# Kernel optimization log

Measured on AMD Instinct MI355X. Metric: run time of the kernel, lower is better.

## Reference

```python
import jax, jax.numpy as jnp
import numpy as np

IN_CH, D, K = 256, 128, 512

def setup_inputs() -> dict:
    key = jax.random.key(0)
    k1, k2, k3, k4 = jax.random.split(key, 4)
    x = jax.random.normal(k1, (16, IN_CH, 64, 64), dtype=jnp.float32)
    W = jax.random.normal(k2, (D, IN_CH), dtype=jnp.float32) * (1.0 / np.sqrt(IN_CH))
    b = jax.random.normal(k3, (D,), dtype=jnp.float32) * 0.01
    prototypes = jax.random.normal(k4, (K, D), dtype=jnp.float32) * 0.02
    gamma = jnp.asarray(1.0, dtype=jnp.float32)
    return {"x": x, "W": W, "b": b, "prototypes": prototypes, "gamma": gamma}

def reference(x, W, b, prototypes, gamma):
    n, c, h, w = x.shape
    # 1x1 conv projection: [n,c,h,w] -> [n,h,w,d]
    q = jnp.einsum('nchw,dc->nhwd', x, W) + b
    q_flat = q.reshape(n * h * w, -1)                      # [T, d]
    q_norm2 = jnp.sum(q_flat * q_flat, axis=1, keepdims=True)   # [T, 1]
    p_norm2 = jnp.sum(prototypes * prototypes, axis=1)[None, :] # [1, K]
    dist2 = q_norm2 + p_norm2 - 2.0 * (q_flat @ prototypes.T)   # [T, K]
    weights = jax.nn.softmax(-jnp.abs(gamma) * dist2, axis=1)
    return weights.reshape(n, h, w, -1).transpose(0, 3, 1, 2)   # [n, K, h, w]
```

## Files before the change

### kernel.cpp

```cpp
#include <hip/hip_runtime.h>

#define HW 4096
#define NCH 256
#define DIM 128
#define NPROTO 512

typedef __attribute__((ext_vector_type(4))) float f32x4;
typedef __attribute__((ext_vector_type(8))) short s16x8;

__device__ __forceinline__ unsigned short f2bf(float f) {
  union { float f; unsigned u; } v; v.f = f;
  unsigned r = v.u + 0x7fffu + ((v.u >> 16) & 1u);
  return (unsigned short)(r >> 16);
}

__device__ __forceinline__ void gload_lds16(const void* g, void* l) {
  __builtin_amdgcn_global_load_lds(
      (const __attribute__((address_space(1))) void*)g,
      (__attribute__((address_space(3))) void*)l, 16, 0, 0);
}

__global__ __launch_bounds__(256) void prep_kernel(const float* __restrict__ P,
                                                   const float* __restrict__ Wm,
                                                   unsigned short* __restrict__ Pbf,
                                                   unsigned short* __restrict__ Wbf,
                                                   float* __restrict__ pn2) {
  const int tid = threadIdx.x;
  const int b = blockIdx.x;
  if (b < 8) {
    const int n  = b * 64 + (tid >> 2);
    const int qt = tid & 3;
    const float* row = P + n * DIM + qt * 32;
    unsigned short* dst = Pbf + (size_t)n * DIM + qt * 32;
    float ssq = 0.f;
#pragma unroll
    for (int u = 0; u < 8; ++u) {
      f32x4 v = *(const f32x4*)(row + 4 * u);
      ssq += v.x * v.x + v.y * v.y + v.z * v.z + v.w * v.w;
      dst[4 * u + 0] = f2bf(v.x);
      dst[4 * u + 1] = f2bf(v.y);
      dst[4 * u + 2] = f2bf(v.z);
      dst[4 * u + 3] = f2bf(v.w);
    }
    ssq += __shfl_xor(ssq, 1);
    ssq += __shfl_xor(ssq, 2);
    if (qt == 0) pn2[n] = ssq;
  } else {
    const int idx = ((b - 8) * 256 + tid) * 16;
#pragma unroll
    for (int u = 0; u < 4; ++u) {
      f32x4 v = *(const f32x4*)(Wm + idx + 4 * u);
      unsigned short* d = Wbf + idx + 4 * u;
      d[0] = f2bf(v.x); d[1] = f2bf(v.y); d[2] = f2bf(v.z); d[3] = f2bf(v.w);
    }
  }
}

__global__ __launch_bounds__(512) void proj_kernel(const float* __restrict__ x,
                                                   const unsigned short* __restrict__ Wbf,
                                                   const float* __restrict__ bias,
                                                   unsigned short* __restrict__ qbf) {
  __shared__ __align__(16) unsigned short x_s[128 * 72];
  __shared__ __align__(16) unsigned short w_s[128 * 64];
  const int tid  = threadIdx.x;
  const int p0   = blockIdx.x * 128;
  const int nimg = p0 >> 12;
  const int hw0  = p0 & 4095;
  const float* xbase = x + (size_t)nimg * NCH * HW + hw0;
  const int wave = tid >> 6, lane = tid & 63;
  const int l15 = lane & 15, l4 = lane >> 4;

  f32x4 acc[8];
#pragma unroll
  for (int j = 0; j < 8; ++j)
#pragma unroll
    for (int r = 0; r < 4; ++r) acc[j][r] = 0.f;

  const int wrow0 = 8 * wave + (lane >> 3);
  const int wc8   = lane & 7;

  for (int c0 = 0; c0 < NCH; c0 += 64) {
#pragma unroll
    for (int t = 0; t < 2; ++t) {
      const int row = 64 * t + wrow0;
      const unsigned short* src =
          Wbf + (size_t)row * NCH + c0 + ((wc8 ^ (row & 7)) << 3);
      gload_lds16(src, (char*)w_s + t * 8192 + wave * 1024);
    }
    {
      const int f = tid & 31, cl = tid >> 5;
#pragma unroll
      for (int r = 0; r < 4; ++r) {
        const int cc = cl + 16 * r;
        f32x4 v = *(const f32x4*)(xbase + (size_t)(c0 + cc) * HW + 4 * f);
        x_s[(4 * f + 0) * 72 + cc] = f2bf(v.x);
        x_s[(4 * f + 1) * 72 + cc] = f2bf(v.y);
        x_s[(4 * f + 2) * 72 + cc] = f2bf(v.z);
        x_s[(4 * f + 3) * 72 + cc] = f2bf(v.w);
      }
    }
    __syncthreads();
#pragma unroll
    for (int kc = 0; kc < 64; kc += 32) {
      s16x8 a = *(const s16x8*)&x_s[(16 * wave + l15) * 72 + kc + 8 * l4];
      const int ub = (kc >> 3) + l4;
#pragma unroll
      for (int j = 0; j < 8; ++j) {
        s16x8 b = *(const s16x8*)&w_s[(16 * j + l15) * 64 + ((ub ^ (l15 & 7)) << 3)];
        acc[j] = __builtin_amdgcn_mfma_f32_16x16x32_bf16(a, b, acc[j], 0, 0, 0);
      }
    }
    __syncthreads();
  }
  const int mb = 16 * wave + 4 * l4;
#pragma unroll
  for (int j = 0; j < 8; ++j) {
    const int d = 16 * j + l15;
    const float bv = bias[d];
#pragma unroll
    for (int r = 0; r < 4; ++r)
      qbf[(size_t)(p0 + mb + r) * DIM + d] = f2bf(acc[j][r] + bv);
  }
}

__global__ __launch_bounds__(256, 4) void attn_kernel(const unsigned short* __restrict__ qbf,
                                                      const unsigned short* __restrict__ Pbf,
                                                      const float* __restrict__ pn2,
                                                      const float* __restrict__ gptr,
                                                      float* __restrict__ out) {
  __shared__ float red[4 * 32];
  __shared__ float rmx[32];
  __shared__ float rinv[32];

  const int tid  = threadIdx.x;
  const int p0   = blockIdx.x * 32;
  const int nimg = p0 >> 12;
  const int hw0  = p0 & 4095;
  const int wv = tid >> 6, lane = tid & 63;
  const int l15 = lane & 15, l4 = lane >> 4;

  const float g2  = fabsf(gptr[0]) * 1.44269504088896340736f;
  const float tg2 = 2.f * g2;

  f32x4 acc[2][8];
#pragma unroll
  for (int i = 0; i < 2; ++i)
#pragma unroll
    for (int j = 0; j < 8; ++j)
#pragma unroll
      for (int r = 0; r < 4; ++r) acc[i][j][r] = 0.f;

  const unsigned short* qrow = qbf + (size_t)(p0 + l15) * DIM + 8 * l4;
  const unsigned short* prow = Pbf + (size_t)(128 * wv + l15) * DIM + 8 * l4;

#pragma unroll
  for (int ch = 0; ch < 4; ++ch) {
    const int dk = 32 * ch;
    s16x8 afr[2];
#pragma unroll
    for (int i = 0; i < 2; ++i)
      afr[i] = *(const s16x8*)(qrow + (size_t)(16 * i) * DIM + dk);
#pragma unroll
    for (int j = 0; j < 8; ++j) {
      s16x8 bfr = *(const s16x8*)(prow + (size_t)(16 * j) * DIM + dk);
#pragma unroll
      for (int i = 0; i < 2; ++i)
        acc[i][j] = __builtin_amdgcn_mfma_f32_16x16x32_bf16(afr[i], bfr, acc[i][j], 0, 0, 0);
    }
  }

  float cj[8];
#pragma unroll
  for (int j = 0; j < 8; ++j) cj[j] = g2 * pn2[128 * wv + 16 * j + l15];

  const int rbase = 4 * l4;

#pragma unroll
  for (int i = 0; i < 2; ++i)
#pragma unroll
    for (int r = 0; r < 4; ++r) {
      float m = -1e30f;
#pragma unroll
      for (int j = 0; j < 8; ++j) {
        float lv = fmaf(acc[i][j][r], tg2, -cj[j]);
        acc[i][j][r] = lv;
        m = fmaxf(m, lv);
      }
#pragma unroll
      for (int s = 1; s < 16; s <<= 1) m = fmaxf(m, __shfl_xor(m, s));
      if (l15 == 0) red[wv * 32 + 16 * i + rbase + r] = m;
    }
  __syncthreads();
  if (tid < 32) {
    float M = red[tid];
#pragma unroll
    for (int w = 1; w < 4; ++w) M = fmaxf(M, red[w * 32 + tid]);
    rmx[tid] = M;
  }
  __syncthreads();

#pragma unroll
  for (int i = 0; i < 2; ++i)
#pragma unroll
    for (int r = 0; r < 4; ++r) {
      const float M = rmx[16 * i + rbase + r];
      float s = 0.f;
#pragma unroll
      for (int j = 0; j < 8; ++j) {
        float e = exp2f(acc[i][j][r] - M);
        acc[i][j][r] = e;
        s += e;
      }
#pragma unroll
      for (int t = 1; t < 16; t <<= 1) s += __shfl_xor(s, t);
      if (l15 == 0) red[wv * 32 + 16 * i + rbase + r] = s;
    }
  __syncthreads();
  if (tid < 32) {
    float S = red[tid] + red[32 + tid] + red[64 + tid] + red[96 + tid];
    rinv[tid] = 1.f / S;
  }
  __syncthreads();

  float inv[2][4];
#pragma unroll
  for (int i = 0; i < 2; ++i)
#pragma unroll
    for (int r = 0; r < 4; ++r) inv[i][r] = rinv[16 * i + rbase + r];

  float* obase = out + (size_t)nimg * NPROTO * HW + hw0;
#pragma unroll
  for (int i = 0; i < 2; ++i) {
    const int px = 16 * i + rbase;
#pragma unroll
    for (int j = 0; j < 8; ++j) {
      const int k = 128 * wv + 16 * j + l15;
      f32x4 o = acc[i][j];
      o.x *= inv[i][0]; o.y *= inv[i][1]; o.z *= inv[i][2]; o.w *= inv[i][3];
      *(f32x4*)(obase + (size_t)k * HW + px) = o;
    }
  }
}

extern "C" void kernel_launch(void* const* d_in, const int* in_sizes, int n_in,
                              void* d_out, int out_size, void* d_ws, size_t ws_size,
                              hipStream_t stream) {
  const float* x     = (const float*)d_in[0];
  const float* Wm    = (const float*)d_in[1];
  const float* bias  = (const float*)d_in[2];
  const float* prot  = (const float*)d_in[3];
  const float* gamma = (const float*)d_in[4];
  float* out = (float*)d_out;

  unsigned short* q_ws  = (unsigned short*)d_ws;
  unsigned short* P_ws  = (unsigned short*)((char*)d_ws + 16777216);
  float*          pn2_w = (float*)((char*)d_ws + 16777216 + 131072);
  unsigned short* W_ws  = (unsigned short*)((char*)d_ws + 16777216 + 131072 + 2048);

  prep_kernel<<<16, 256, 0, stream>>>(prot, Wm, P_ws, W_ws, pn2_w);
  proj_kernel<<<512, 512, 0, stream>>>(x, W_ws, bias, q_ws);
  attn_kernel<<<2048, 256, 0, stream>>>(q_ws, P_ws, pn2_w, gamma, out);
}
```

Before: 250.9 us.

## Fuse projection and prototype softmax into one kernel via register shuffles

Merges the projection GEMM and the distance/softmax kernel into a single kernel where each wave handles 16 pixels across all 512 prototypes. The projected q values stay in registers and are transposed into MFMA operand layout with lane shuffles, which removes the bf16 q round trip through global memory and one launch. Softmax reductions become wave-local, so shared memory and block barriers are no longer needed. In exchange, W and prototype fragments are read straight from global/L2 with no LDS reuse, the kernel holds large accumulator register arrays (acc2 of 32 f32x4), and output stores are scalar and strided by HW.

Result: slower. 311.4 us (+24.1%).

```diff
diff --git a/kernel.cpp b/kernel.cpp
--- a/kernel.cpp
+++ b/kernel.cpp
@@ -7,6 +7,7 @@
 
 typedef __attribute__((ext_vector_type(4))) float f32x4;
 typedef __attribute__((ext_vector_type(8))) short s16x8;
+typedef __attribute__((ext_vector_type(4))) unsigned u32x4;
 
 __device__ __forceinline__ unsigned short f2bf(float f) {
   union { float f; unsigned u; } v; v.f = f;
@@ -14,10 +15,10 @@
   return (unsigned short)(r >> 16);
 }
 
-__device__ __forceinline__ void gload_lds16(const void* g, void* l) {
-  __builtin_amdgcn_global_load_lds(
-      (const __attribute__((address_space(1))) void*)g,
-      (__attribute__((address_space(3))) void*)l, 16, 0, 0);
+__device__ __forceinline__ unsigned cvt_pk_bf16(float lo, float hi) {
+  unsigned d;
+  asm("v_cvt_pk_bf16_f32 %0, %1, %2" : "=v"(d) : "v"(lo), "v"(hi));
+  return d;
 }
 
 __global__ __launch_bounds__(256) void prep_kernel(const float* __restrict__ P,
@@ -56,190 +57,128 @@
   }
 }
 
-__global__ __launch_bounds__(512) void proj_kernel(const float* __restrict__ x,
-                                                   const unsigned short* __restrict__ Wbf,
-                                                   const float* __restrict__ bias,
-                                                   unsigned short* __restrict__ qbf) {
-  __shared__ __align__(16) unsigned short x_s[128 * 72];
-  __shared__ __align__(16) unsigned short w_s[128 * 64];
+__global__ __launch_bounds__(128, 2) void fused_kernel(
+    const float* __restrict__ x, const unsigned short* __restrict__ Wbf,
+    const float* __restrict__ bias, const unsigned short* __restrict__ Pbf,
+    const float* __restrict__ pn2, const float* __restrict__ gptr,
+    float* __restrict__ out) {
   const int tid  = threadIdx.x;
-  const int p0   = blockIdx.x * 128;
-  const int nimg = p0 >> 12;
-  const int hw0  = p0 & 4095;
-  const float* xbase = x + (size_t)nimg * NCH * HW + hw0;
-  const int wave = tid >> 6, lane = tid & 63;
-  const int l15 = lane & 15, l4 = lane >> 4;
-
-  f32x4 acc[8];
-#pragma unroll
-  for (int j = 0; j < 8; ++j)
-#pragma unroll
-    for (int r = 0; r < 4; ++r) acc[j][r] = 0.f;
-
-  const int wrow0 = 8 * wave + (lane >> 3);
-  const int wc8   = lane & 7;
-
-  for (int c0 = 0; c0 < NCH; c0 += 64) {
-#pragma unroll
-    for (int t = 0; t < 2; ++t) {
-      const int row = 64 * t + wrow0;
-      const unsigned short* src =
-          Wbf + (size_t)row * NCH + c0 + ((wc8 ^ (row & 7)) << 3);
-      gload_lds16(src, (char*)w_s + t * 8192 + wave * 1024);
-    }
-    {
-      const int f = tid & 31, cl = tid >> 5;
-#pragma unroll
-      for (int r = 0; r < 4; ++r) {
-        const int cc = cl + 16 * r;
-        f32x4 v = *(const f32x4*)(xbase + (size_t)(c0 + cc) * HW + 4 * f);
-        x_s[(4 * f + 0) * 72 + cc] = f2bf(v.x);
-        x_s[(4 * f + 1) * 72 + cc] = f2bf(v.y);
-        x_s[(4 * f + 2) * 72 + cc] = f2bf(v.z);
-        x_s[(4 * f + 3) * 72 + cc] = f2bf(v.w);
-      }
-    }
-    __syncthreads();
-#pragma unroll
-    for (int kc = 0; kc < 64; kc += 32) {
-      s16x8 a = *(const s16x8*)&x_s[(16 * wave + l15) * 72 + kc + 8 * l4];
-      const int ub = (kc >> 3) + l4;
-#pragma unroll
-      for (int j = 0; j < 8; ++j) {
-        s16x8 b = *(const s16x8*)&w_s[(16 * j + l15) * 64 + ((ub ^ (l15 & 7)) << 3)];
-        acc[j] = __builtin_amdgcn_mfma_f32_16x16x32_bf16(a, b, acc[j], 0, 0, 0);
-      }
-    }
-    __syncthreads();
-  }
-  const int mb = 16 * wave + 4 * l4;
-#pragma unroll
-  for (int j = 0; j < 8; ++j) {
-    const int d = 16 * j + l15;
-    const float bv = bias[d];
-#pragma unroll
-    for (int r = 0; r < 4; ++r)
-      qbf[(size_t)(p0 + mb + r) * DIM + d] = f2bf(acc[j][r] + bv);
-  }
-}
-
-__global__ __launch_bounds__(256, 4) void attn_kernel(const unsigned short* __restrict__ qbf,
-                                                      const unsigned short* __restrict__ Pbf,
-                                                      const float* __restrict__ pn2,
-                                                      const float* __restrict__ gptr,
-                                                      float* __restrict__ out) {
-  __shared__ float red[4 * 32];
-  __shared__ float rmx[32];
-  __shared__ float rinv[32];
-
-  const int tid  = threadIdx.x;
+  const int wv   = tid >> 6, lane = tid & 63;
+  const int l15  = lane & 15, l4 = lane >> 4;
   const int p0   = blockIdx.x * 32;
   const int nimg = p0 >> 12;
-  const int hw0  = p0 & 4095;
-  const int wv = tid >> 6, lane = tid & 63;
-  const int l15 = lane & 15, l4 = lane >> 4;
+  const int hw   = (p0 & 4095) + 16 * wv + l15;
+
+  const float* xb = x + (size_t)nimg * NCH * HW + hw;
+
+  f32x4 acc1[8];
+#pragma unroll
+  for (int t = 0; t < 8; ++t)
+#pragma unroll
+    for (int r = 0; r < 4; ++r) acc1[t][r] = 0.f;
+
+#pragma unroll
+  for (int s = 0; s < 8; ++s) {
+    float xr[8];
+#pragma unroll
+    for (int j = 0; j < 8; ++j)
+      xr[j] = xb[(size_t)(32 * s + 8 * l4 + j) * HW];
+    u32x4 bxu;
+#pragma unroll
+    for (int p = 0; p < 4; ++p)
+      bxu[p] = cvt_pk_bf16(xr[2 * p], xr[2 * p + 1]);
+    s16x8 bx = __builtin_bit_cast(s16x8, bxu);
+#pragma unroll
+    for (int t = 0; t < 8; ++t) {
+      s16x8 aw = *(const s16x8*)(Wbf + (size_t)(16 * t + l15) * NCH + 32 * s + 8 * l4);
+      acc1[t] = __builtin_amdgcn_mfma_f32_16x16x32_bf16(aw, bx, acc1[t], 0, 0, 0);
+    }
+  }
+
+#pragma unroll
+  for (int t = 0; t < 8; ++t) {
+    f32x4 bv = *(const f32x4*)(bias + 16 * t + 4 * l4);
+#pragma unroll
+    for (int r = 0; r < 4; ++r) acc1[t][r] += bv[r];
+  }
+
+  unsigned pk[8][2];
+#pragma unroll
+  for (int t = 0; t < 8; ++t)
+#pragma unroll
+    for (int pr = 0; pr < 2; ++pr)
+      pk[t][pr] = cvt_pk_bf16(acc1[t][2 * pr], acc1[t][2 * pr + 1]);
+
+  u32x4 qBu[4];
+#pragma unroll
+  for (int c = 0; c < 4; ++c)
+#pragma unroll
+    for (int p = 0; p < 4; ++p) {
+      const int sl = l15 + 16 * (2 * (l4 & 1) + (p >> 1));
+      unsigned va = (unsigned)__shfl((int)pk[2 * c + 0][p & 1], sl);
+      unsigned vb = (unsigned)__shfl((int)pk[2 * c + 1][p & 1], sl);
+      qBu[c][p] = (l4 >> 1) ? vb : va;
+    }
+
+  f32x4 acc2[32];
+#pragma unroll
+  for (int T = 0; T < 32; ++T)
+#pragma unroll
+    for (int r = 0; r < 4; ++r) acc2[T][r] = 0.f;
+
+  const s16x8 qB0 = __builtin_bit_cast(s16x8, qBu[0]);
+  const s16x8 qB1 = __builtin_bit_cast(s16x8, qBu[1]);
+  const s16x8 qB2 = __builtin_bit_cast(s16x8, qBu[2]);
+  const s16x8 qB3 = __builtin_bit_cast(s16x8, qBu[3]);
+
+#pragma unroll
+  for (int T = 0; T < 32; ++T) {
+    const unsigned short* pr = Pbf + (size_t)(16 * T + l15) * DIM + 8 * l4;
+    s16x8 a0 = *(const s16x8*)(pr + 0);
+    s16x8 a1 = *(const s16x8*)(pr + 32);
+    s16x8 a2 = *(const s16x8*)(pr + 64);
+    s16x8 a3 = *(const s16x8*)(pr + 96);
+    acc2[T] = __builtin_amdgcn_mfma_f32_16x16x32_bf16(a0, qB0, acc2[T], 0, 0, 0);
+    acc2[T] = __builtin_amdgcn_mfma_f32_16x16x32_bf16(a1, qB1, acc2[T], 0, 0, 0);
+    acc2[T] = __builtin_amdgcn_mfma_f32_16x16x32_bf16(a2, qB2, acc2[T], 0, 0, 0);
+    acc2[T] = __builtin_amdgcn_mfma_f32_16x16x32_bf16(a3, qB3, acc2[T], 0, 0, 0);
+  }
 
   const float g2  = fabsf(gptr[0]) * 1.44269504088896340736f;
   const float tg2 = 2.f * g2;
 
-  f32x4 acc[2][8];
-#pragma unroll
-  for (int i = 0; i < 2; ++i)
-#pragma unroll
-    for (int j = 0; j < 8; ++j)
-#pragma unroll
-      for (int r = 0; r < 4; ++r) acc[i][j][r] = 0.f;
-
-  const unsigned short* qrow = qbf + (size_t)(p0 + l15) * DIM + 8 * l4;
-  const unsigned short* prow = Pbf + (size_t)(128 * wv + l15) * DIM + 8 * l4;
-
-#pragma unroll
-  for (int ch = 0; ch < 4; ++ch) {
-    const int dk = 32 * ch;
-    s16x8 afr[2];
-#pragma unroll
-    for (int i = 0; i < 2; ++i)
-      afr[i] = *(const s16x8*)(qrow + (size_t)(16 * i) * DIM + dk);
-#pragma unroll
-    for (int j = 0; j < 8; ++j) {
-      s16x8 bfr = *(const s16x8*)(prow + (size_t)(16 * j) * DIM + dk);
-#pragma unroll
-      for (int i = 0; i < 2; ++i)
-        acc[i][j] = __builtin_amdgcn_mfma_f32_16x16x32_bf16(afr[i], bfr, acc[i][j], 0, 0, 0);
-    }
-  }
-
-  float cj[8];
-#pragma unroll
-  for (int j = 0; j < 8; ++j) cj[j] = g2 * pn2[128 * wv + 16 * j + l15];
-
-  const int rbase = 4 * l4;
-
-#pragma unroll
-  for (int i = 0; i < 2; ++i)
+  float m = -1e30f;
+#pragma unroll
+  for (int T = 0; T < 32; ++T) {
+    f32x4 pv = *(const f32x4*)(pn2 + 16 * T + 4 * l4);
 #pragma unroll
     for (int r = 0; r < 4; ++r) {
-      float m = -1e30f;
-#pragma unroll
-      for (int j = 0; j < 8; ++j) {
-        float lv = fmaf(acc[i][j][r], tg2, -cj[j]);
-        acc[i][j][r] = lv;
-        m = fmaxf(m, lv);
-      }
-#pragma unroll
-      for (int s = 1; s < 16; s <<= 1) m = fmaxf(m, __shfl_xor(m, s));
-      if (l15 == 0) red[wv * 32 + 16 * i + rbase + r] = m;
-    }
-  __syncthreads();
-  if (tid < 32) {
-    float M = red[tid];
-#pragma unroll
-    for (int w = 1; w < 4; ++w) M = fmaxf(M, red[w * 32 + tid]);
-    rmx[tid] = M;
-  }
-  __syncthreads();
-
-#pragma unroll
-  for (int i = 0; i < 2; ++i)
+      acc2[T][r] = fmaf(acc2[T][r], tg2, -g2 * pv[r]);
+      m = fmaxf(m, acc2[T][r]);
+    }
+  }
+  m = fmaxf(m, __shfl_xor(m, 16));
+  m = fmaxf(m, __shfl_xor(m, 32));
+
+  float ssum = 0.f;
+#pragma unroll
+  for (int T = 0; T < 32; ++T)
 #pragma unroll
     for (int r = 0; r < 4; ++r) {
-      const float M = rmx[16 * i + rbase + r];
-      float s = 0.f;
-#pragma unroll
-      for (int j = 0; j < 8; ++j) {
-        float e = exp2f(acc[i][j][r] - M);
-        acc[i][j][r] = e;
-        s += e;
-      }
-#pragma unroll
-      for (int t = 1; t < 16; t <<= 1) s += __shfl_xor(s, t);
-      if (l15 == 0) red[wv * 32 + 16 * i + rbase + r] = s;
-    }
-  __syncthreads();
-  if (tid < 32) {
-    float S = red[tid] + red[32 + tid] + red[64 + tid] + red[96 + tid];
-    rinv[tid] = 1.f / S;
-  }
-  __syncthreads();
-
-  float inv[2][4];
-#pragma unroll
-  for (int i = 0; i < 2; ++i)
-#pragma unroll
-    for (int r = 0; r < 4; ++r) inv[i][r] = rinv[16 * i + rbase + r];
-
-  float* obase = out + (size_t)nimg * NPROTO * HW + hw0;
-#pragma unroll
-  for (int i = 0; i < 2; ++i) {
-    const int px = 16 * i + rbase;
-#pragma unroll
-    for (int j = 0; j < 8; ++j) {
-      const int k = 128 * wv + 16 * j + l15;
-      f32x4 o = acc[i][j];
-      o.x *= inv[i][0]; o.y *= inv[i][1]; o.z *= inv[i][2]; o.w *= inv[i][3];
-      *(f32x4*)(obase + (size_t)k * HW + px) = o;
-    }
-  }
+      float e = exp2f(acc2[T][r] - m);
+      acc2[T][r] = e;
+      ssum += e;
+    }
+  ssum += __shfl_xor(ssum, 16);
+  ssum += __shfl_xor(ssum, 32);
+  const float inv = 1.f / ssum;
+
+  float* ob = out + (size_t)nimg * NPROTO * HW + ((p0 & 4095) + 16 * wv + l15);
+#pragma unroll
+  for (int T = 0; T < 32; ++T)
+#pragma unroll
+    for (int r = 0; r < 4; ++r)
+      ob[(size_t)(16 * T + 4 * l4 + r) * HW] = acc2[T][r] * inv;
 }
 
 extern "C" void kernel_launch(void* const* d_in, const int* in_sizes, int n_in,
@@ -252,12 +191,10 @@
   const float* gamma = (const float*)d_in[4];
   float* out = (float*)d_out;
 
-  unsigned short* q_ws  = (unsigned short*)d_ws;
-  unsigned short* P_ws  = (unsigned short*)((char*)d_ws + 16777216);
-  float*          pn2_w = (float*)((char*)d_ws + 16777216 + 131072);
-  unsigned short* W_ws  = (unsigned short*)((char*)d_ws + 16777216 + 131072 + 2048);
+  unsigned short* P_ws  = (unsigned short*)d_ws;
+  float*          pn2_w = (float*)((char*)d_ws + 131072);
+  unsigned short* W_ws  = (unsigned short*)((char*)d_ws + 131072 + 2048);
 
   prep_kernel<<<16, 256, 0, stream>>>(prot, Wm, P_ws, W_ws, pn2_w);
-  proj_kernel<<<512, 512, 0, stream>>>(x, W_ws, bias, q_ws);
-  attn_kernel<<<2048, 256, 0, stream>>>(q_ws, P_ws, pn2_w, gamma, out);
-}
+  fused_kernel<<<2048, 128, 0, stream>>>(x, W_ws, bias, P_ws, pn2_w, gamma, out);
+}
```
